# Kernel tuning notes

Measured on AMD Instinct MI355X. Metric: run time of the kernel, lower is better.

Reference implementation:

```python
import jax, jax.numpy as jnp
import numpy as np

N, E, B = 100000, 1600000, 64
TD, VD, AD = 768, 2048, 512
HC, H = 32, 4
NV, NA = 20000, 20000


def setup_inputs() -> dict:
    key = jax.random.key(0)
    ks = iter(jax.random.split(key, 80))
    def nrm(shape, scale=0.05):
        return (jax.random.normal(next(ks), shape, jnp.float32) * scale)
    inp = {}
    inp["x"] = jax.random.normal(next(ks), (N, TD), jnp.float32)
    inp["x_vision"] = jax.random.normal(next(ks), (NV, VD), jnp.float32)
    inp["x_audio"] = jax.random.normal(next(ks), (NA, AD), jnp.float32)
    inp["src"] = jax.random.randint(next(ks), (E,), 0, N, jnp.int32)
    inp["dst"] = jax.random.randint(next(ks), (E,), 0, N, jnp.int32)
    inp["vidx"] = jnp.arange(NV, dtype=jnp.int32) + 1000   # disjoint vision node ids
    inp["aidx"] = jnp.arange(NA, dtype=jnp.int32) + 30000  # disjoint audio node ids
    inp["ptr"] = (jnp.arange(B + 1) * (N // B)).astype(jnp.int32)
    # modality projections
    inp["Wt"] = nrm((HC, TD)); inp["bt"] = jnp.zeros((HC,), jnp.float32)
    inp["Wv"] = nrm((HC, VD)); inp["bv"] = jnp.zeros((HC,), jnp.float32)
    inp["gv"] = jnp.ones((HC,), jnp.float32); inp["bev"] = jnp.zeros((HC,), jnp.float32)
    inp["Wa"] = nrm((HC, AD)); inp["ba"] = jnp.zeros((HC,), jnp.float32)
    inp["ga"] = jnp.ones((HC,), jnp.float32); inp["bea"] = jnp.zeros((HC,), jnp.float32)
    # GATv2 convs: (in_dim, heads, concat)
    for p, cin, h, concat in (("c1", HC, H, True), ("c2", HC * H, H, True), ("c3", HC * H, H, True), ("c4", HC * H, 1, False)):
        inp[p + "_Wl"] = nrm((h * HC, cin)); inp[p + "_bl"] = jnp.zeros((h * HC,), jnp.float32)
        inp[p + "_Wr"] = nrm((h * HC, cin)); inp[p + "_br"] = jnp.zeros((h * HC,), jnp.float32)
        inp[p + "_att"] = nrm((h, HC))
        inp[p + "_b"] = jnp.zeros((h * HC if concat else HC,), jnp.float32)
    # layer norms
    for p, d in (("n1", HC * H), ("n2", HC * H), ("n3", HC * H), ("n4", HC)):
        inp[p + "_g"] = jnp.ones((d,), jnp.float32); inp[p + "_b"] = jnp.zeros((d,), jnp.float32)
    inp["Wo"] = nrm((1, HC), 0.01); inp["bo"] = jnp.zeros((1,), jnp.float32)
    return inp


def layernorm(x, g, b):
    m = x.mean(-1, keepdims=True)
    v = x.var(-1, keepdims=True)
    return (x - m) / jnp.sqrt(v + 1e-5) * g + b


def gatv2(x, src, dst, Wl, bl, Wr, br, att, b, concat):
    # PyG GATv2Conv (share_weights=False): e = att . leaky_relu(xl[src] + xr[dst])
    n = x.shape[0]
    h, c = att.shape
    xl = (x @ Wl.T + bl).reshape(n, h, c)
    xr = (x @ Wr.T + br).reshape(n, h, c)
    e = jnp.einsum('ehc,hc->eh', jax.nn.leaky_relu(xl[src] + xr[dst], 0.2), att)
    m = jax.ops.segment_max(e, dst, num_segments=n)          # segment softmax over dst
    w = jnp.exp(e - m[dst])
    s = jax.ops.segment_sum(w, dst, num_segments=n)
    alpha = w / (s[dst] + 1e-16)
    out = jax.ops.segment_sum(alpha[:, :, None] * xl[src], dst, num_segments=n)
    out = out.reshape(n, h * c) if concat else out.mean(1)
    return out + b


def reference(x, x_vision, x_audio, Wt, bt, Wv, bv, gv, bev, Wa, ba, ga, bea,
              c1_Wl, c1_bl, c1_Wr, c1_br, c1_att, c1_b,
              c2_Wl, c2_bl, c2_Wr, c2_br, c2_att, c2_b,
              c3_Wl, c3_bl, c3_Wr, c3_br, c3_att, c3_b,
              c4_Wl, c4_bl, c4_Wr, c4_br, c4_att, c4_b,
              n1_g, n1_b, n2_g, n2_b, n3_g, n3_b, n4_g, n4_b, Wo, bo,
              src, dst, vidx, aidx, ptr):
    n = x.shape[0]
    sl = jnp.arange(n, dtype=src.dtype)  # add_self_loops=True
    s2 = jnp.concatenate([src, sl]); d2 = jnp.concatenate([dst, sl])
    fx = x @ Wt.T + bt  # text projection (dropout = identity in eval)
    hv = jax.nn.relu(layernorm(x_vision @ Wv.T + bv, gv, bev))
    fx = fx.at[vidx].set(hv * x[vidx].mean(1, keepdims=True))
    ha = jax.nn.relu(layernorm(x_audio @ Wa.T + ba, ga, bea))
    fx = fx.at[aidx].set(ha * x[aidx].mean(1, keepdims=True))
    h1 = jax.nn.elu(layernorm(gatv2(fx, s2, d2, c1_Wl, c1_bl, c1_Wr, c1_br, c1_att, c1_b, True), n1_g, n1_b))
    h2 = jax.nn.elu(layernorm(gatv2(h1, s2, d2, c2_Wl, c2_bl, c2_Wr, c2_br, c2_att, c2_b, True) + h1, n2_g, n2_b))
    h3 = jax.nn.elu(layernorm(gatv2(h2, s2, d2, c3_Wl, c3_bl, c3_Wr, c3_br, c3_att, c3_b, True) + h2, n3_g, n3_b))
    h4 = layernorm(gatv2(h3, s2, d2, c4_Wl, c4_bl, c4_Wr, c4_br, c4_att, c4_b, False), n4_g, n4_b)
    summary = h4[ptr[:-1]]  # summary node = first node of each graph
    out = (summary @ Wo.T + bo).squeeze(-1)  # num_classes==2 -> squeeze
    return out
```

## Files before the change

### kernel.cpp

```cpp
#include <hip/hip_runtime.h>
#include <math.h>

#define NND 100000
#define NED 1600000
#define TDIM 768
#define VDIM 2048
#define ADIM 512
#define NVV 20000
#define NAA 20000
#define NBB 64
#define SUBROWS 8192

static __device__ __forceinline__ unsigned short f2bf(float f) {
  unsigned int u = __float_as_uint(f);
  unsigned int r = (u + 0x7fffu + ((u >> 16) & 1u)) >> 16;
  return (unsigned short)r;
}
static __device__ __forceinline__ float bf2f(unsigned int s) {
  return __uint_as_float(s << 16);
}

typedef __attribute__((ext_vector_type(8))) short bfrag;
typedef __attribute__((ext_vector_type(4))) float facc4;

static __device__ __forceinline__ bfrag pack8(const float4& a, const float4& b) {
  union { bfrag v; unsigned short u[8]; } r;
  r.u[0] = f2bf(a.x); r.u[1] = f2bf(a.y); r.u[2] = f2bf(a.z); r.u[3] = f2bf(a.w);
  r.u[4] = f2bf(b.x); r.u[5] = f2bf(b.y); r.u[6] = f2bf(b.z); r.u[7] = f2bf(b.w);
  return r.v;
}

static __device__ __forceinline__ float red16(float v) {
  #pragma unroll
  for (int m = 8; m >= 1; m >>= 1) v += __shfl_xor(v, m, 64);
  return v;
}
static __device__ __forceinline__ float red32(float v) {
  #pragma unroll
  for (int m = 16; m >= 1; m >>= 1) v += __shfl_xor(v, m, 64);
  return v;
}

__global__ void k_setcnt(int* cnt, int n) {
  int i = blockIdx.x * 256 + threadIdx.x;
  if (i < n) cnt[i] = 1;
}
__global__ void k_count(const int* __restrict__ dst, int* cnt, int e) {
  int i = blockIdx.x * 256 + threadIdx.x;
  if (i < e) atomicAdd(&cnt[dst[i]], 1);
}
__global__ void k_scan1(const int* __restrict__ cnt, int* rp, int* bsum, int n) {
  __shared__ int lds[256];
  int t = threadIdx.x;
  int base = blockIdx.x * 1024;
  int v[4];
  int s = 0;
  #pragma unroll
  for (int j = 0; j < 4; ++j) {
    int i = base + t * 4 + j;
    int c = (i < n) ? cnt[i] : 0;
    s += c; v[j] = s;
  }
  lds[t] = s;
  __syncthreads();
  for (int ofs = 1; ofs < 256; ofs <<= 1) {
    int x = (t >= ofs) ? lds[t - ofs] : 0;
    __syncthreads();
    lds[t] += x;
    __syncthreads();
  }
  int excl = (t > 0) ? lds[t - 1] : 0;
  #pragma unroll
  for (int j = 0; j < 4; ++j) {
    int i = base + t * 4 + j;
    if (i < n) rp[i + 1] = excl + v[j];
  }
  if (t == 255) bsum[blockIdx.x] = lds[255];
}
__global__ void k_scan2(int* bsum, int nb) {
  if (threadIdx.x == 0 && blockIdx.x == 0) {
    int acc = 0;
    for (int b = 0; b < nb; ++b) { int t = bsum[b]; bsum[b] = acc; acc += t; }
  }
}
__global__ void k_scan3(int* rp, const int* __restrict__ bsum, int n) {
  int i = blockIdx.x * 256 + threadIdx.x;
  if (i < n) rp[i + 1] += bsum[i >> 10];
  if (i == 0) rp[0] = 0;
}
__global__ void k_fillself(const int* __restrict__ rp, int* colidx, int* fill, int n) {
  int i = blockIdx.x * 256 + threadIdx.x;
  if (i < n) { colidx[rp[i]] = i; fill[i] = 1; }
}
__global__ void k_filledge(const int* __restrict__ src, const int* __restrict__ dst,
                           const int* __restrict__ rp, int* fill, int* colidx, int e) {
  int i = blockIdx.x * 256 + threadIdx.x;
  if (i < e) {
    int d = dst[i];
    int p = atomicAdd(&fill[d], 1);
    colidx[rp[d] + p] = src[i];
  }
}

__global__ void k_zeromark(int* m3, int* m2, int* cnts, int n) {
  int i = blockIdx.x * 256 + threadIdx.x;
  if (i < n) { m3[i] = 0; m2[i] = 0; }
  if (i < 2) cnts[i] = 0;
}
__global__ void k_mark3(const int* __restrict__ ptr, const int* __restrict__ rp,
                        const int* __restrict__ colidx, int* mark) {
  int node = ptr[blockIdx.x];
  int eb = rp[node], ee = rp[node + 1];
  if (threadIdx.x == 0) mark[node] = 1;
  for (int e = eb + (int)threadIdx.x; e < ee; e += 256) mark[colidx[e]] = 1;
}
__global__ void k_mark2(const int* __restrict__ list3, const int* __restrict__ cnt3,
                        const int* __restrict__ rp, const int* __restrict__ colidx,
                        int* mark) {
  int n3 = *cnt3;
  int wid = (blockIdx.x * 256 + threadIdx.x) >> 6;
  int l = threadIdx.x & 63;
  int nw = gridDim.x * 4;
  for (int i = wid; i < n3; i += nw) {
    int node = list3[i];
    if (l == 0) mark[node] = 1;
    int eb = rp[node], ee = rp[node + 1];
    for (int e = eb + l; e < ee; e += 64) mark[colidx[e]] = 1;
  }
}
__global__ void k_compact(const int* __restrict__ mark, int* list, int* cnt, int n) {
  int i = blockIdx.x * 256 + threadIdx.x;
  if (i < n && mark[i]) {
    int p = atomicAdd(cnt, 1);
    list[p] = i;
  }
}

__global__ void k_packall(
    const float* __restrict__ W0l, const float* __restrict__ W0r, unsigned short* o0,
    const float* __restrict__ W1l, const float* __restrict__ W1r, unsigned short* o1,
    const float* __restrict__ W2l, const float* __restrict__ W2r, unsigned short* o2,
    const float* __restrict__ W3l, const float* __restrict__ W3r, unsigned short* o3,
    const float* __restrict__ Wt, unsigned short* ot,
    const float* __restrict__ Wv, unsigned short* ov,
    const float* __restrict__ Wa, unsigned short* oa) {
  int i = blockIdx.x * 256 + threadIdx.x;
  if (i < 4096) { o0[i] = f2bf(W0l[i]); o0[4096 + i] = f2bf(W0r[i]); return; }
  i -= 4096;
  if (i < 16384) { o1[i] = f2bf(W1l[i]); o1[16384 + i] = f2bf(W1r[i]); return; }
  i -= 16384;
  if (i < 16384) { o2[i] = f2bf(W2l[i]); o2[16384 + i] = f2bf(W2r[i]); return; }
  i -= 16384;
  if (i < 4096) { o3[i] = f2bf(W3l[i]); o3[4096 + i] = f2bf(W3r[i]); return; }
  i -= 4096;
  if (i < 24576) { ot[i] = f2bf(Wt[i]); return; }
  i -= 24576;
  if (i < 65536) { ov[i] = f2bf(Wv[i]); return; }
  i -= 65536;
  if (i < 16384) { oa[i] = f2bf(Wa[i]); return; }
}

template <int K, bool MEAN, bool OBF>
__global__ __launch_bounds__(256) void gemm_mfma_in(
    const float* __restrict__ A, const unsigned short* __restrict__ Wb,
    const float* __restrict__ bias, void* __restrict__ Cv,
    float* __restrict__ rowmean, int M) {
  constexpr int KT = K / 32;
  const int wid = (int)threadIdx.x >> 6;
  const int lane = (int)threadIdx.x & 63;
  const int r16 = lane & 15;
  const int kg = lane >> 4;
  const int m0 = (blockIdx.x * 4 + wid) * 16;
  if (m0 >= M) return;
  const float* arow = A + (size_t)(m0 + r16) * K + kg * 8;
  const unsigned short* w0 = Wb + (size_t)r16 * K + kg * 8;
  const unsigned short* w1 = Wb + (size_t)(16 + r16) * K + kg * 8;
  facc4 acc0 = (facc4){0.f, 0.f, 0.f, 0.f};
  facc4 acc1 = (facc4){0.f, 0.f, 0.f, 0.f};
  float msum = 0.f;
  #pragma unroll 4
  for (int kt = 0; kt < KT; ++kt) {
    const float4* ap = reinterpret_cast<const float4*>(arow + kt * 32);
    float4 a0 = ap[0], a1 = ap[1];
    if (MEAN) msum += (a0.x + a0.y + a0.z + a0.w) + (a1.x + a1.y + a1.z + a1.w);
    bfrag af = pack8(a0, a1);
    bfrag b0 = *reinterpret_cast<const bfrag*>(w0 + kt * 32);
    bfrag b1 = *reinterpret_cast<const bfrag*>(w1 + kt * 32);
    acc0 = __builtin_amdgcn_mfma_f32_16x16x32_bf16(af, b0, acc0, 0, 0, 0);
    acc1 = __builtin_amdgcn_mfma_f32_16x16x32_bf16(af, b1, acc1, 0, 0, 0);
  }
  float b0v = bias[r16], b1v = bias[16 + r16];
  #pragma unroll
  for (int r = 0; r < 4; ++r) {
    int rowg = m0 + kg * 4 + r;
    float v0 = acc0[r] + b0v, v1 = acc1[r] + b1v;
    if (OBF) {
      unsigned short* C = (unsigned short*)Cv;
      C[(size_t)rowg * 32 + r16] = f2bf(v0);
      C[(size_t)rowg * 32 + 16 + r16] = f2bf(v1);
    } else {
      float* C = (float*)Cv;
      C[(size_t)rowg * 32 + r16] = v0;
      C[(size_t)rowg * 32 + 16 + r16] = v1;
    }
  }
  if (MEAN) {
    msum += __shfl_xor(msum, 16, 64);
    msum += __shfl_xor(msum, 32, 64);
    if (lane < 16) rowmean[m0 + r16] = msum * (1.f / (float)K);
  }
}

template <int K, int NHALF, int WAVES, bool IDX>
__global__ __launch_bounds__(WAVES * 64) void gemm_mfma(
    const unsigned short* __restrict__ A,
    const unsigned short* __restrict__ Wb,
    const float* __restrict__ bl, const float* __restrict__ br,
    unsigned short* __restrict__ Cl, unsigned short* __restrict__ Cr, int M,
    const int* __restrict__ rows, const int* __restrict__ rcnt) {
  constexpr int KT = K / 32;
  constexpr int NT = 2 * NHALF / 16;
  constexpr int NPW = NT / WAVES;
  static_assert(NPW >= 1, "bad wave split");
  const int wid = (int)threadIdx.x >> 6;
  const int lane = (int)threadIdx.x & 63;
  const int r16 = lane & 15;
  const int kg = lane >> 4;
  const int m0 = blockIdx.x * 16;
  int nr = M;
  if (IDX) nr = *rcnt;
  if (m0 >= nr) return;
  bfrag bf[NPW][KT];
  #pragma unroll
  for (int n = 0; n < NPW; ++n) {
    int col = (wid * NPW + n) * 16 + r16;
    #pragma unroll
    for (int kt = 0; kt < KT; ++kt)
      bf[n][kt] = *reinterpret_cast<const bfrag*>(Wb + (size_t)col * K + kt * 32 + kg * 8);
  }
  int ra = m0 + r16;
  if (IDX) { int mm = ra < nr ? ra : nr - 1; ra = rows[mm]; }
  bfrag af[KT];
  const unsigned short* arow = A + (size_t)ra * K + kg * 8;
  #pragma unroll
  for (int kt = 0; kt < KT; ++kt)
    af[kt] = *reinterpret_cast<const bfrag*>(arow + kt * 32);
  facc4 acc[NPW];
  #pragma unroll
  for (int n = 0; n < NPW; ++n) acc[n] = (facc4){0.f, 0.f, 0.f, 0.f};
  #pragma unroll
  for (int kt = 0; kt < KT; ++kt)
    #pragma unroll
    for (int n = 0; n < NPW; ++n)
      acc[n] = __builtin_amdgcn_mfma_f32_16x16x32_bf16(af[kt], bf[n][kt], acc[n], 0, 0, 0);
  #pragma unroll
  for (int n = 0; n < NPW; ++n) {
    int colg = (wid * NPW + n) * 16 + r16;
    bool isL = colg < NHALF;
    float bias = isL ? bl[colg] : br[colg - NHALF];
    #pragma unroll
    for (int r = 0; r < 4; ++r) {
      int m = m0 + kg * 4 + r;
      if (IDX && m >= nr) continue;
      int rowg = IDX ? rows[m] : m;
      unsigned short v = f2bf(acc[n][r] + bias);
      if (isL) Cl[(size_t)rowg * NHALF + colg] = v;
      else     Cr[(size_t)rowg * NHALF + (colg - NHALF)] = v;
    }
  }
}

template <bool RES, bool WL>
__global__ __launch_bounds__(256) void gat_agg_post128(
    const unsigned short* __restrict__ xl, const unsigned short* __restrict__ xr,
    const float* __restrict__ att,
    const int* __restrict__ rp, const int* __restrict__ colidx,
    const float* __restrict__ cb, const unsigned short* res,
    const float* __restrict__ g, const float* __restrict__ b,
    unsigned short* __restrict__ out, int n,
    const int* __restrict__ wl, const int* __restrict__ wcnt) {
  int wid = (blockIdx.x * 256 + threadIdx.x) >> 6;
  int node;
  if (WL) {
    if (wid >= *wcnt) return;
    node = wl[wid];
  } else {
    if (wid >= n) return;
    node = wid;
  }
  const int base = node * 128;
  int l = threadIdx.x & 63;
  const int lh = l & 31;
  const int half = l >> 5;
  const int c4 = 4 * lh;
  float4 a = *reinterpret_cast<const float4*>(att + c4);
  uint2 xru = *reinterpret_cast<const uint2*>(xr + base + c4);
  float xr0 = bf2f(xru.x & 0xffffu), xr1 = bf2f(xru.x >> 16);
  float xr2 = bf2f(xru.y & 0xffffu), xr3 = bf2f(xru.y >> 16);
  float m_ = -1e30f, s_ = 0.f;
  float ac0 = 0.f, ac1 = 0.f, ac2 = 0.f, ac3 = 0.f;
  int eb = rp[node], ee = rp[node + 1];
  int cnt = ee - eb;
  int nstep = (cnt + 1) >> 1;

  auto step = [&](uint2 cur, bool go) {
    float x0 = bf2f(cur.x & 0xffffu), x1 = bf2f(cur.x >> 16);
    float x2 = bf2f(cur.y & 0xffffu), x3 = bf2f(cur.y >> 16);
    float z0 = x0 + xr0, z1 = x1 + xr1, z2 = x2 + xr2, z3 = x3 + xr3;
    float t = (z0 > 0.f ? z0 : 0.2f * z0) * a.x + (z1 > 0.f ? z1 : 0.2f * z1) * a.y
            + (z2 > 0.f ? z2 : 0.2f * z2) * a.z + (z3 > 0.f ? z3 : 0.2f * z3) * a.w;
    t += __shfl_xor(t, 1, 64);
    t += __shfl_xor(t, 2, 64);
    t += __shfl_xor(t, 4, 64);
    if (!go) t = -1e30f;
    if (__any(t > m_ + 4.0f)) {
      float nm = fmaxf(m_, t);
      float p = __expf(m_ - nm);
      float w = __expf(t - nm);
      s_ = s_ * p + w;
      ac0 = ac0 * p + w * x0; ac1 = ac1 * p + w * x1;
      ac2 = ac2 * p + w * x2; ac3 = ac3 * p + w * x3;
      m_ = nm;
    } else {
      float w = __expf(t - m_);
      s_ += w;
      ac0 = fmaf(w, x0, ac0); ac1 = fmaf(w, x1, ac1);
      ac2 = fmaf(w, x2, ac2); ac3 = fmaf(w, x3, ac3);
    }
  };
  auto eclamp = [&](int s) { int e = 2 * s + half; return eb + (e < cnt ? e : cnt - 1); };
  auto ldx = [&](int sn) {
    return *reinterpret_cast<const uint2*>(xl + (size_t)sn * 128 + c4);
  };

  int idx[4];
  uint2 pv[4];
  #pragma unroll
  for (int k = 0; k < 4; ++k) idx[k] = colidx[eclamp(k)];
  #pragma unroll
  for (int k = 0; k < 4; ++k) pv[k] = ldx(idx[k]);
  for (int i = 0; i < nstep; i += 4) {
    uint2 q[4];
    #pragma unroll
    for (int k = 0; k < 4; ++k) q[k] = pv[k];
    if (i + 4 < nstep) {
      #pragma unroll
      for (int k = 0; k < 4; ++k) idx[k] = colidx[eclamp(i + 4 + k)];
      #pragma unroll
      for (int k = 0; k < 4; ++k) pv[k] = ldx(idx[k]);
    }
    step(q[0], 2 * i + half < cnt);
    if (i + 1 < nstep) step(q[1], 2 * (i + 1) + half < cnt);
    if (i + 2 < nstep) step(q[2], 2 * (i + 2) + half < cnt);
    if (i + 3 < nstep) step(q[3], 2 * (i + 3) + half < cnt);
  }

  float om = __shfl_xor(m_, 32, 64);
  float os = __shfl_xor(s_, 32, 64);
  float oa0 = __shfl_xor(ac0, 32, 64);
  float oa1 = __shfl_xor(ac1, 32, 64);
  float oa2 = __shfl_xor(ac2, 32, 64);
  float oa3 = __shfl_xor(ac3, 32, 64);
  float nm = fmaxf(m_, om);
  float ps = __expf(m_ - nm), po = __expf(om - nm);
  float s = s_ * ps + os * po;
  float inv = 1.f / (s + 1e-16f);
  float4 cbv = *reinterpret_cast<const float4*>(cb + c4);
  float v0 = (ac0 * ps + oa0 * po) * inv + cbv.x;
  float v1 = (ac1 * ps + oa1 * po) * inv + cbv.y;
  float v2 = (ac2 * ps + oa2 * po) * inv + cbv.z;
  float v3 = (ac3 * ps + oa3 * po) * inv + cbv.w;
  if (RES) {
    uint2 rv = *reinterpret_cast<const uint2*>(res + base + c4);
    v0 += bf2f(rv.x & 0xffffu); v1 += bf2f(rv.x >> 16);
    v2 += bf2f(rv.y & 0xffffu); v3 += bf2f(rv.y >> 16);
  }
  float S = v0 + v1 + v2 + v3;
  float Q = v0 * v0 + v1 * v1 + v2 * v2 + v3 * v3;
  #pragma unroll
  for (int m = 16; m >= 1; m >>= 1) {
    S += __shfl_xor(S, m, 64);
    Q += __shfl_xor(Q, m, 64);
  }
  float mean = S * (1.f / 128.f);
  float var = Q * (1.f / 128.f) - mean * mean;
  float rstd = rsqrtf(var + 1e-5f);
  float4 gv = *reinterpret_cast<const float4*>(g + c4);
  float4 bv = *reinterpret_cast<const float4*>(b + c4);
  float y0 = (v0 - mean) * rstd * gv.x + bv.x;
  float y1 = (v1 - mean) * rstd * gv.y + bv.y;
  float y2 = (v2 - mean) * rstd * gv.z + bv.z;
  float y3 = (v3 - mean) * rstd * gv.w + bv.w;
  y0 = (y0 > 0.f) ? y0 : expm1f(y0);
  y1 = (y1 > 0.f) ? y1 : expm1f(y1);
  y2 = (y2 > 0.f) ? y2 : expm1f(y2);
  y3 = (y3 > 0.f) ? y3 : expm1f(y3);
  if (half == 0) {
    uint2 o;
    o.x = (unsigned int)f2bf(y0) | ((unsigned int)f2bf(y1) << 16);
    o.y = (unsigned int)f2bf(y2) | ((unsigned int)f2bf(y3) << 16);
    *reinterpret_cast<uint2*>(out + base + c4) = o;
  }
}

__global__ void k_prep4(const int* __restrict__ ptr, const int* __restrict__ rp,
                        const int* __restrict__ colidx, int* off, int* gidx) {
  __shared__ int cnt_s[64];
  __shared__ int off_s[65];
  int t = threadIdx.x;
  if (t < 64) {
    int node = ptr[t];
    int deg = rp[node + 1] - rp[node];
    if (deg > 126) deg = 126;
    cnt_s[t] = deg + 1;
  }
  __syncthreads();
  if (t == 0) {
    int acc = 0;
    for (int i = 0; i < 64; ++i) { off_s[i] = acc; acc += cnt_s[i]; }
    off_s[64] = acc;
  }
  __syncthreads();
  if (t < 65) off[t] = off_s[t];
  if (t < 64) {
    int node = ptr[t];
    int o = off_s[t];
    gidx[o] = node;
    int eb = rp[node];
    int deg = cnt_s[t] - 1;
    for (int j = 0; j < deg; ++j) gidx[o + 1 + j] = colidx[eb + j];
  }
}

__global__ void k_gath4(const unsigned short* __restrict__ h, const int* __restrict__ gidx,
                        const int* __restrict__ off, unsigned short* __restrict__ hsub) {
  int tid = blockIdx.x * 256 + threadIdx.x;
  int j = tid >> 4, q = tid & 15;
  if (j >= SUBROWS) return;
  int count = off[64];
  bfrag v;
  #pragma unroll
  for (int i = 0; i < 8; ++i) v[i] = 0;
  if (j < count) v = *reinterpret_cast<const bfrag*>(h + (size_t)gidx[j] * 128 + q * 8);
  *reinterpret_cast<bfrag*>(hsub + (size_t)j * 128 + q * 8) = v;
}

__global__ __launch_bounds__(256) void k_agg4_final(
    const unsigned short* __restrict__ xls, const unsigned short* __restrict__ xrs,
    const float* __restrict__ att, const int* __restrict__ off,
    const float* __restrict__ cb, const float* __restrict__ g,
    const float* __restrict__ b, const float* __restrict__ Wo,
    const float* __restrict__ bo, float* __restrict__ out) {
  int wid = (blockIdx.x * 256 + threadIdx.x) >> 6;
  int l = threadIdx.x & 63;
  int lg = l & 15;
  int node = 4 * wid + (l >> 4);
  int c2 = 2 * lg;
  int p0 = off[node], pe = off[node + 1];
  int deg = pe - p0 - 1;
  float2 a = *reinterpret_cast<const float2*>(att + c2);
  unsigned int xru = *reinterpret_cast<const unsigned int*>(xrs + (size_t)p0 * 32 + c2);
  float xr0 = bf2f(xru & 0xffffu), xr1 = bf2f(xru >> 16);
  float m_ = -1e30f, s_ = 0.f, accx = 0.f, accy = 0.f;
  for (int i = 0;; ++i) {
    bool go = i < deg;
    if (!__any(go)) break;
    float xcx = 0.f, xcy = 0.f;
    float t = -1e30f;
    if (go) {
      unsigned int pv = *reinterpret_cast<const unsigned int*>(xls + (size_t)(p0 + 1 + i) * 32 + c2);
      xcx = bf2f(pv & 0xffffu);
      xcy = bf2f(pv >> 16);
      float z0 = xcx + xr0, z1 = xcy + xr1;
      t = (z0 > 0.f ? z0 : 0.2f * z0) * a.x + (z1 > 0.f ? z1 : 0.2f * z1) * a.y;
    }
    t = red16(t);
    if (!go) t = -1e30f;
    if (__any(t > m_ + 4.0f)) {
      float nm = fmaxf(m_, t);
      float p = __expf(m_ - nm);
      float w = __expf(t - nm);
      s_ = s_ * p + w;
      accx = accx * p + w * xcx;
      accy = accy * p + w * xcy;
      m_ = nm;
    } else {
      float w = __expf(t - m_);
      s_ += w;
      accx = fmaf(w, xcx, accx);
      accy = fmaf(w, xcy, accy);
    }
  }
  float inv = 1.f / (s_ + 1e-16f);
  float2 cbv = *reinterpret_cast<const float2*>(cb + c2);
  float v0 = accx * inv + cbv.x;
  float v1 = accy * inv + cbv.y;
  float S = red16(v0 + v1);
  float Q = red16(v0 * v0 + v1 * v1);
  float mean = S * (1.f / 32.f);
  float var = Q * (1.f / 32.f) - mean * mean;
  float rstd = rsqrtf(var + 1e-5f);
  float2 gv = *reinterpret_cast<const float2*>(g + c2);
  float2 bv = *reinterpret_cast<const float2*>(b + c2);
  float y0 = (v0 - mean) * rstd * gv.x + bv.x;
  float y1 = (v1 - mean) * rstd * gv.y + bv.y;
  float2 wo = *reinterpret_cast<const float2*>(Wo + c2);
  float d = red16(y0 * wo.x + y1 * wo.y);
  if (lg == 0) out[node] = d + bo[0];
}

__global__ __launch_bounds__(256) void k_modal2(
    unsigned short* fx, const float* __restrict__ hv, const float* __restrict__ ha,
    const int* __restrict__ vidx, const int* __restrict__ aidx,
    const float* __restrict__ gv, const float* __restrict__ bev,
    const float* __restrict__ ga, const float* __restrict__ bea,
    const float* __restrict__ rowmean, int nv, int na) {
  int wid = (blockIdx.x * 256 + threadIdx.x) >> 6;
  int l = threadIdx.x & 63;
  if (wid >= nv + na) return;
  bool isV = wid < nv;
  int w2 = isV ? wid : wid - nv;
  const float* hraw = isV ? hv : ha;
  const float* gg = isV ? gv : ga;
  const float* be = isV ? bev : bea;
  int node = isV ? vidx[w2] : aidx[w2];
  float mean = rowmean[node];
  float hval = (l < 32) ? hraw[(size_t)w2 * 32 + l] : 0.f;
  float S = red32(hval);
  float Q = red32(hval * hval);
  if (l < 32) {
    float m2 = S * (1.f / 32.f);
    float var = Q * (1.f / 32.f) - m2 * m2;
    float rstd = rsqrtf(var + 1e-5f);
    float y = (hval - m2) * rstd * gg[l] + be[l];
    y = fmaxf(y, 0.f);
    fx[(size_t)node * 32 + l] = f2bf(y * mean);
  }
}

extern "C" void kernel_launch(void* const* d_in, const int* in_sizes, int n_in,
                              void* d_out, int out_size, void* d_ws, size_t ws_size,
                              hipStream_t stream) {
  const float* x   = (const float*)d_in[0];
  const float* xv  = (const float*)d_in[1];
  const float* xa  = (const float*)d_in[2];
  const int* src   = (const int*)d_in[3];
  const int* dst   = (const int*)d_in[4];
  const int* vidx  = (const int*)d_in[5];
  const int* aidx  = (const int*)d_in[6];
  const int* ptr   = (const int*)d_in[7];
  const float* Wt  = (const float*)d_in[8];
  const float* bt  = (const float*)d_in[9];
  const float* Wv  = (const float*)d_in[10];
  const float* bv  = (const float*)d_in[11];
  const float* gv  = (const float*)d_in[12];
  const float* bev = (const float*)d_in[13];
  const float* Wa  = (const float*)d_in[14];
  const float* ba  = (const float*)d_in[15];
  const float* ga  = (const float*)d_in[16];
  const float* bea = (const float*)d_in[17];
  const float* cW_l[4], *cb_l[4], *cW_r[4], *cb_r[4], *c_att[4], *c_b[4];
  for (int i = 0; i < 4; ++i) {
    cW_l[i]  = (const float*)d_in[18 + 6 * i + 0];
    cb_l[i]  = (const float*)d_in[18 + 6 * i + 1];
    cW_r[i]  = (const float*)d_in[18 + 6 * i + 2];
    cb_r[i]  = (const float*)d_in[18 + 6 * i + 3];
    c_att[i] = (const float*)d_in[18 + 6 * i + 4];
    c_b[i]   = (const float*)d_in[18 + 6 * i + 5];
  }
  const float* ng[4], *nb_[4];
  for (int i = 0; i < 4; ++i) {
    ng[i]  = (const float*)d_in[42 + 2 * i + 0];
    nb_[i] = (const float*)d_in[42 + 2 * i + 1];
  }
  const float* Wo = (const float*)d_in[50];
  const float* bo = (const float*)d_in[51];
  float* out = (float*)d_out;

  char* w = (char*)d_ws;
  auto alloc = [&](size_t bytes) {
    char* p = w;
    w += (bytes + 255) & ~(size_t)255;
    return p;
  };
  int* rowptr = (int*)alloc((NND + 1) * sizeof(int));
  int* cnt    = (int*)alloc(NND * sizeof(int));
  int* bsum   = (int*)alloc(1024 * sizeof(int));
  int* colidx = (int*)alloc((size_t)(NED + NND) * sizeof(int));
  float* rowmean = (float*)alloc((size_t)NND * sizeof(float));
  unsigned short* fx = (unsigned short*)alloc((size_t)NND * 32 * sizeof(unsigned short));
  unsigned short* h  = (unsigned short*)alloc((size_t)NND * 128 * sizeof(unsigned short));
  unsigned short* xlb = (unsigned short*)alloc((size_t)NND * 128 * sizeof(unsigned short));
  unsigned short* xrb = (unsigned short*)alloc((size_t)NND * 128 * sizeof(unsigned short));
  float* hvraw = (float*)alloc((size_t)NVV * 32 * sizeof(float));
  float* haraw = (float*)alloc((size_t)NAA * 32 * sizeof(float));
  unsigned short* wb0 = (unsigned short*)alloc(256 * 32 * sizeof(unsigned short));
  unsigned short* wb1 = (unsigned short*)alloc(256 * 128 * sizeof(unsigned short));
  unsigned short* wb2 = (unsigned short*)alloc(256 * 128 * sizeof(unsigned short));
  unsigned short* wb3 = (unsigned short*)alloc(64 * 128 * sizeof(unsigned short));
  unsigned short* wbt = (unsigned short*)alloc(32 * TDIM * sizeof(unsigned short));
  unsigned short* wbv = (unsigned short*)alloc(32 * VDIM * sizeof(unsigned short));
  unsigned short* wba = (unsigned short*)alloc(32 * ADIM * sizeof(unsigned short));
  int* off4 = (int*)alloc(65 * sizeof(int));
  int* gidx = (int*)alloc(SUBROWS * sizeof(int));
  unsigned short* hsub = (unsigned short*)alloc((size_t)SUBROWS * 128 * sizeof(unsigned short));
  unsigned short* xls = (unsigned short*)alloc((size_t)SUBROWS * 32 * sizeof(unsigned short));
  unsigned short* xrs = (unsigned short*)alloc((size_t)SUBROWS * 32 * sizeof(unsigned short));
  int* mark3 = (int*)alloc((size_t)NND * sizeof(int));
  int* mark2 = (int*)alloc((size_t)NND * sizeof(int));
  int* list3 = (int*)alloc((size_t)NND * sizeof(int));
  int* list2 = (int*)alloc((size_t)NND * sizeof(int));
  int* cnts  = (int*)alloc(2 * sizeof(int));

  const int nblk_n = (NND + 255) / 256;
  const int nblk_e = (NED + 255) / 256;
  const int nscan = (NND + 1023) / 1024;
  const int nwave_n = (NND * 64 + 255) / 256;
  const int nwave_m2 = ((NVV + NAA) * 64 + 255) / 256;
  const int ntile = (NND + 15) / 16;

  k_setcnt<<<nblk_n, 256, 0, stream>>>(cnt, NND);
  k_count<<<nblk_e, 256, 0, stream>>>(dst, cnt, NED);
  k_scan1<<<nscan, 256, 0, stream>>>(cnt, rowptr, bsum, NND);
  k_scan2<<<1, 64, 0, stream>>>(bsum, nscan);
  k_scan3<<<nblk_n, 256, 0, stream>>>(rowptr, bsum, NND);
  k_fillself<<<nblk_n, 256, 0, stream>>>(rowptr, colidx, cnt, NND);
  k_filledge<<<nblk_e, 256, 0, stream>>>(src, dst, rowptr, cnt, colidx, NED);

  k_packall<<<576, 256, 0, stream>>>(
      cW_l[0], cW_r[0], wb0, cW_l[1], cW_r[1], wb1,
      cW_l[2], cW_r[2], wb2, cW_l[3], cW_r[3], wb3,
      Wt, wbt, Wv, wbv, Wa, wba);

  k_prep4<<<1, 256, 0, stream>>>(ptr, rowptr, colidx, off4, gidx);

  k_zeromark<<<nblk_n, 256, 0, stream>>>(mark3, mark2, cnts, NND);
  k_mark3<<<64, 256, 0, stream>>>(ptr, rowptr, colidx, mark3);
  k_compact<<<nblk_n, 256, 0, stream>>>(mark3, list3, cnts + 0, NND);
  k_mark2<<<256, 256, 0, stream>>>(list3, cnts + 0, rowptr, colidx, mark2);
  k_compact<<<nblk_n, 256, 0, stream>>>(mark2, list2, cnts + 1, NND);

  gemm_mfma_in<TDIM, true, true><<<(NND + 63) / 64, 256, 0, stream>>>(
      x, wbt, bt, fx, rowmean, NND);
  gemm_mfma_in<VDIM, false, false><<<(NVV + 63) / 64, 256, 0, stream>>>(
      xv, wbv, bv, hvraw, nullptr, NVV);
  gemm_mfma_in<ADIM, false, false><<<(NAA + 63) / 64, 256, 0, stream>>>(
      xa, wba, ba, haraw, nullptr, NAA);
  k_modal2<<<nwave_m2, 256, 0, stream>>>(
      fx, hvraw, haraw, vidx, aidx, gv, bev, ga, bea, rowmean, NVV, NAA);

  gemm_mfma<32, 128, 8, false><<<ntile, 512, 0, stream>>>(
      fx, wb0, cb_l[0], cb_r[0], xlb, xrb, NND, nullptr, nullptr);
  gat_agg_post128<false, false><<<nwave_n, 256, 0, stream>>>(
      xlb, xrb, c_att[0], rowptr, colidx, c_b[0], nullptr, ng[0], nb_[0], h, NND,
      nullptr, nullptr);

  gemm_mfma<128, 128, 8, false><<<ntile, 512, 0, stream>>>(
      h, wb1, cb_l[1], cb_r[1], xlb, xrb, NND, nullptr, nullptr);
  gat_agg_post128<true, true><<<nwave_n, 256, 0, stream>>>(
      xlb, xrb, c_att[1], rowptr, colidx, c_b[1], h, ng[1], nb_[1], h, NND,
      list2, cnts + 1);

  gemm_mfma<128, 128, 8, true><<<ntile, 512, 0, stream>>>(
      h, wb2, cb_l[2], cb_r[2], xlb, xrb, NND, list2, cnts + 1);
  gat_agg_post128<true, true><<<nwave_n, 256, 0, stream>>>(
      xlb, xrb, c_att[2], rowptr, colidx, c_b[2], h, ng[2], nb_[2], h, NND,
      list3, cnts + 0);

  k_gath4<<<(SUBROWS * 16 + 255) / 256, 256, 0, stream>>>(h, gidx, off4, hsub);
  gemm_mfma<128, 32, 4, false><<<SUBROWS / 16, 256, 0, stream>>>(
      hsub, wb3, cb_l[3], cb_r[3], xls, xrs, SUBROWS, nullptr, nullptr);
  k_agg4_final<<<4, 256, 0, stream>>>(
      xls, xrs, c_att[3], off4, c_b[3], ng[3], nb_[3], Wo, bo, out);
}
```

Baseline: 673.0 us.

## Fuse preprocessing kernels, single-pass scan, merged input GEMMs, gather-free layer-4 GEMM

```diff
diff --git a/kernel.cpp b/kernel.cpp
--- a/kernel.cpp
+++ b/kernel.cpp
@@ -11,6 +11,14 @@
 #define NBB 64
 #define SUBROWS 8192
 
+#define NBLK_N ((NND + 255) / 256)
+#define NBLK_E ((NED + 255) / 256)
+#define NSCAN ((NND + 1023) / 1024)
+#define NPACK 576
+#define NT_TXT ((NND + 63) / 64)
+#define NT_VIS ((NVV + 63) / 64)
+#define NT_AUD ((NAA + 63) / 64)
+
 static __device__ __forceinline__ unsigned short f2bf(float f) {
   unsigned int u = __float_as_uint(f);
   unsigned int r = (u + 0x7fffu + ((u >> 16) & 1u)) >> 16;
@@ -41,102 +49,15 @@
   return v;
 }
 
-__global__ void k_setcnt(int* cnt, int n) {
+__global__ void k_init(int* cnt, int* fill, int* m3, int* m2, int* cnts, int* agg, int n) {
   int i = blockIdx.x * 256 + threadIdx.x;
-  if (i < n) cnt[i] = 1;
-}
-__global__ void k_count(const int* __restrict__ dst, int* cnt, int e) {
-  int i = blockIdx.x * 256 + threadIdx.x;
-  if (i < e) atomicAdd(&cnt[dst[i]], 1);
-}
-__global__ void k_scan1(const int* __restrict__ cnt, int* rp, int* bsum, int n) {
-  __shared__ int lds[256];
-  int t = threadIdx.x;
-  int base = blockIdx.x * 1024;
-  int v[4];
-  int s = 0;
-  #pragma unroll
-  for (int j = 0; j < 4; ++j) {
-    int i = base + t * 4 + j;
-    int c = (i < n) ? cnt[i] : 0;
-    s += c; v[j] = s;
-  }
-  lds[t] = s;
-  __syncthreads();
-  for (int ofs = 1; ofs < 256; ofs <<= 1) {
-    int x = (t >= ofs) ? lds[t - ofs] : 0;
-    __syncthreads();
-    lds[t] += x;
-    __syncthreads();
-  }
-  int excl = (t > 0) ? lds[t - 1] : 0;
-  #pragma unroll
-  for (int j = 0; j < 4; ++j) {
-    int i = base + t * 4 + j;
-    if (i < n) rp[i + 1] = excl + v[j];
-  }
-  if (t == 255) bsum[blockIdx.x] = lds[255];
-}
-__global__ void k_scan2(int* bsum, int nb) {
-  if (threadIdx.x == 0 && blockIdx.x == 0) {
-    int acc = 0;
-    for (int b = 0; b < nb; ++b) { int t = bsum[b]; bsum[b] = acc; acc += t; }
-  }
-}
-__global__ void k_scan3(int* rp, const int* __restrict__ bsum, int n) {
-  int i = blockIdx.x * 256 + threadIdx.x;
-  if (i < n) rp[i + 1] += bsum[i >> 10];
-  if (i == 0) rp[0] = 0;
-}
-__global__ void k_fillself(const int* __restrict__ rp, int* colidx, int* fill, int n) {
-  int i = blockIdx.x * 256 + threadIdx.x;
-  if (i < n) { colidx[rp[i]] = i; fill[i] = 1; }
-}
-__global__ void k_filledge(const int* __restrict__ src, const int* __restrict__ dst,
-                           const int* __restrict__ rp, int* fill, int* colidx, int e) {
-  int i = blockIdx.x * 256 + threadIdx.x;
-  if (i < e) {
-    int d = dst[i];
-    int p = atomicAdd(&fill[d], 1);
-    colidx[rp[d] + p] = src[i];
-  }
-}
-
-__global__ void k_zeromark(int* m3, int* m2, int* cnts, int n) {
-  int i = blockIdx.x * 256 + threadIdx.x;
-  if (i < n) { m3[i] = 0; m2[i] = 0; }
+  if (i < n) { cnt[i] = 1; fill[i] = 1; m3[i] = 0; m2[i] = 0; }
   if (i < 2) cnts[i] = 0;
-}
-__global__ void k_mark3(const int* __restrict__ ptr, const int* __restrict__ rp,
-                        const int* __restrict__ colidx, int* mark) {
-  int node = ptr[blockIdx.x];
-  int eb = rp[node], ee = rp[node + 1];
-  if (threadIdx.x == 0) mark[node] = 1;
-  for (int e = eb + (int)threadIdx.x; e < ee; e += 256) mark[colidx[e]] = 1;
-}
-__global__ void k_mark2(const int* __restrict__ list3, const int* __restrict__ cnt3,
-                        const int* __restrict__ rp, const int* __restrict__ colidx,
-                        int* mark) {
-  int n3 = *cnt3;
-  int wid = (blockIdx.x * 256 + threadIdx.x) >> 6;
-  int l = threadIdx.x & 63;
-  int nw = gridDim.x * 4;
-  for (int i = wid; i < n3; i += nw) {
-    int node = list3[i];
-    if (l == 0) mark[node] = 1;
-    int eb = rp[node], ee = rp[node + 1];
-    for (int e = eb + l; e < ee; e += 64) mark[colidx[e]] = 1;
-  }
-}
-__global__ void k_compact(const int* __restrict__ mark, int* list, int* cnt, int n) {
-  int i = blockIdx.x * 256 + threadIdx.x;
-  if (i < n && mark[i]) {
-    int p = atomicAdd(cnt, 1);
-    list[p] = i;
-  }
-}
-
-__global__ void k_packall(
+  if (i < 128) agg[i] = 0;
+}
+
+__global__ void k_cntpack(
+    const int* __restrict__ dst, int* cnt,
     const float* __restrict__ W0l, const float* __restrict__ W0r, unsigned short* o0,
     const float* __restrict__ W1l, const float* __restrict__ W1r, unsigned short* o1,
     const float* __restrict__ W2l, const float* __restrict__ W2r, unsigned short* o2,
@@ -144,7 +65,13 @@
     const float* __restrict__ Wt, unsigned short* ot,
     const float* __restrict__ Wv, unsigned short* ov,
     const float* __restrict__ Wa, unsigned short* oa) {
-  int i = blockIdx.x * 256 + threadIdx.x;
+  int bid = blockIdx.x;
+  if (bid < NBLK_E) {
+    int i = bid * 256 + threadIdx.x;
+    if (i < NED) atomicAdd(&cnt[dst[i]], 1);
+    return;
+  }
+  int i = (bid - NBLK_E) * 256 + threadIdx.x;
   if (i < 4096) { o0[i] = f2bf(W0l[i]); o0[4096 + i] = f2bf(W0r[i]); return; }
   i -= 4096;
   if (i < 16384) { o1[i] = f2bf(W1l[i]); o1[16384 + i] = f2bf(W1r[i]); return; }
@@ -160,17 +87,127 @@
   if (i < 16384) { oa[i] = f2bf(Wa[i]); return; }
 }
 
+__global__ void k_scanall(const int* __restrict__ cnt, int* rp, int* agg, int n) {
+  __shared__ int lds[256];
+  int t = threadIdx.x, b = blockIdx.x;
+  int base = b * 1024;
+  int v[4];
+  int s = 0;
+  #pragma unroll
+  for (int j = 0; j < 4; ++j) {
+    int i = base + t * 4 + j;
+    int c = (i < n) ? cnt[i] : 0;
+    s += c; v[j] = s;
+  }
+  lds[t] = s;
+  __syncthreads();
+  for (int ofs = 1; ofs < 256; ofs <<= 1) {
+    int x = (t >= ofs) ? lds[t - ofs] : 0;
+    __syncthreads();
+    lds[t] += x;
+    __syncthreads();
+  }
+  int excl = (t > 0) ? lds[t - 1] : 0;
+  int total = lds[255];
+  if (t == 0) atomicExch(&agg[b], total);
+  __syncthreads();
+  int psum = 0;
+  for (int j = t; j < b; j += 256) {
+    int a;
+    do { a = atomicAdd(&agg[j], 0); } while (a == 0);
+    psum += a;
+  }
+  lds[t] = psum;
+  __syncthreads();
+  for (int ofs = 128; ofs >= 1; ofs >>= 1) {
+    if (t < ofs) lds[t] += lds[t + ofs];
+    __syncthreads();
+  }
+  int prefix = lds[0];
+  #pragma unroll
+  for (int j = 0; j < 4; ++j) {
+    int i = base + t * 4 + j;
+    if (i < n) rp[i + 1] = prefix + excl + v[j];
+  }
+  if (b == 0 && t == 0) rp[0] = 0;
+}
+
+__global__ void k_fill(const int* __restrict__ src, const int* __restrict__ dst,
+                       const int* __restrict__ rp, int* fill, int* colidx, int n, int e) {
+  int i = blockIdx.x * 256 + threadIdx.x;
+  if (i < n) colidx[rp[i]] = i;
+  if (i < e) {
+    int d = dst[i];
+    int p = atomicAdd(&fill[d], 1);
+    colidx[rp[d] + p] = src[i];
+  }
+}
+
+__global__ void k_prep4m(const int* __restrict__ ptr, const int* __restrict__ rp,
+                         const int* __restrict__ colidx, int* off, int* gidx, int* mark3) {
+  if (blockIdx.x > 0) {
+    int node = ptr[blockIdx.x - 1];
+    int eb = rp[node], ee = rp[node + 1];
+    if (threadIdx.x == 0) mark3[node] = 1;
+    for (int e = eb + (int)threadIdx.x; e < ee; e += 256) mark3[colidx[e]] = 1;
+    return;
+  }
+  __shared__ int cnt_s[64];
+  __shared__ int off_s[65];
+  int t = threadIdx.x;
+  if (t < 64) {
+    int node = ptr[t];
+    int deg = rp[node + 1] - rp[node];
+    if (deg > 126) deg = 126;
+    cnt_s[t] = deg + 1;
+  }
+  __syncthreads();
+  if (t == 0) {
+    int acc = 0;
+    for (int i = 0; i < 64; ++i) { off_s[i] = acc; acc += cnt_s[i]; }
+    off_s[64] = acc;
+  }
+  __syncthreads();
+  if (t < 65) off[t] = off_s[t];
+  if (t < 64) {
+    int node = ptr[t];
+    int o = off_s[t];
+    gidx[o] = node;
+    int eb = rp[node];
+    int deg = cnt_s[t] - 1;
+    for (int j = 0; j < deg; ++j) gidx[o + 1 + j] = colidx[eb + j];
+  }
+}
+
+__global__ void k_mark2s(const int* __restrict__ mark3, const int* __restrict__ rp,
+                         const int* __restrict__ colidx, int* mark2, int n) {
+  int i = blockIdx.x * 256 + threadIdx.x;
+  if (i >= n || !mark3[i]) return;
+  mark2[i] = 1;
+  int eb = rp[i], ee = rp[i + 1];
+  for (int e = eb; e < ee; ++e) mark2[colidx[e]] = 1;
+}
+
+__global__ void k_compact2(const int* __restrict__ m3, const int* __restrict__ m2,
+                           int* l3, int* l2, int* cnts, int n) {
+  int i = blockIdx.x * 256 + threadIdx.x;
+  if (i < n) {
+    if (m3[i]) { int p = atomicAdd(&cnts[0], 1); l3[p] = i; }
+    if (m2[i]) { int p = atomicAdd(&cnts[1], 1); l2[p] = i; }
+  }
+}
+
 template <int K, bool MEAN, bool OBF>
-__global__ __launch_bounds__(256) void gemm_mfma_in(
+static __device__ __forceinline__ void gemm_in_body(
     const float* __restrict__ A, const unsigned short* __restrict__ Wb,
     const float* __restrict__ bias, void* __restrict__ Cv,
-    float* __restrict__ rowmean, int M) {
+    float* __restrict__ rowmean, int M, int bid) {
   constexpr int KT = K / 32;
   const int wid = (int)threadIdx.x >> 6;
   const int lane = (int)threadIdx.x & 63;
   const int r16 = lane & 15;
   const int kg = lane >> 4;
-  const int m0 = (blockIdx.x * 4 + wid) * 16;
+  const int m0 = (bid * 4 + wid) * 16;
   if (m0 >= M) return;
   const float* arow = A + (size_t)(m0 + r16) * K + kg * 8;
   const unsigned short* w0 = Wb + (size_t)r16 * K + kg * 8;
@@ -211,7 +248,24 @@
   }
 }
 
-template <int K, int NHALF, int WAVES, bool IDX>
+__global__ __launch_bounds__(256) void k_gemm_in_all(
+    const float* __restrict__ x, const unsigned short* __restrict__ wbt,
+    const float* __restrict__ bt, unsigned short* fx, float* rowmean,
+    const float* __restrict__ xv, const unsigned short* __restrict__ wbv,
+    const float* __restrict__ bv, float* hvraw,
+    const float* __restrict__ xa, const unsigned short* __restrict__ wba,
+    const float* __restrict__ ba, float* haraw) {
+  int bid = blockIdx.x;
+  if (bid < NT_TXT) {
+    gemm_in_body<TDIM, true, true>(x, wbt, bt, fx, rowmean, NND, bid);
+  } else if (bid < NT_TXT + NT_VIS) {
+    gemm_in_body<VDIM, false, false>(xv, wbv, bv, hvraw, nullptr, NVV, bid - NT_TXT);
+  } else {
+    gemm_in_body<ADIM, false, false>(xa, wba, ba, haraw, nullptr, NAA, bid - NT_TXT - NT_VIS);
+  }
+}
+
+template <int K, int NHALF, int WAVES, int MODE>
 __global__ __launch_bounds__(WAVES * 64) void gemm_mfma(
     const unsigned short* __restrict__ A,
     const unsigned short* __restrict__ Wb,
@@ -228,7 +282,7 @@
   const int kg = lane >> 4;
   const int m0 = blockIdx.x * 16;
   int nr = M;
-  if (IDX) nr = *rcnt;
+  if (MODE >= 1) nr = *rcnt;
   if (m0 >= nr) return;
   bfrag bf[NPW][KT];
   #pragma unroll
@@ -239,7 +293,7 @@
       bf[n][kt] = *reinterpret_cast<const bfrag*>(Wb + (size_t)col * K + kt * 32 + kg * 8);
   }
   int ra = m0 + r16;
-  if (IDX) { int mm = ra < nr ? ra : nr - 1; ra = rows[mm]; }
+  if (MODE >= 1) { int mm = ra < nr ? ra : nr - 1; ra = rows[mm]; }
   bfrag af[KT];
   const unsigned short* arow = A + (size_t)ra * K + kg * 8;
   #pragma unroll
@@ -261,8 +315,8 @@
     #pragma unroll
     for (int r = 0; r < 4; ++r) {
       int m = m0 + kg * 4 + r;
-      if (IDX && m >= nr) continue;
-      int rowg = IDX ? rows[m] : m;
+      if (MODE == 1 && m >= nr) continue;
+      int rowg = (MODE == 1) ? rows[m] : m;
       unsigned short v = f2bf(acc[n][r] + bias);
       if (isL) Cl[(size_t)rowg * NHALF + colg] = v;
       else     Cr[(size_t)rowg * NHALF + (colg - NHALF)] = v;
@@ -401,48 +455,6 @@
     o.y = (unsigned int)f2bf(y2) | ((unsigned int)f2bf(y3) << 16);
     *reinterpret_cast<uint2*>(out + base + c4) = o;
   }
-}
-
-__global__ void k_prep4(const int* __restrict__ ptr, const int* __restrict__ rp,
-                        const int* __restrict__ colidx, int* off, int* gidx) {
-  __shared__ int cnt_s[64];
-  __shared__ int off_s[65];
-  int t = threadIdx.x;
-  if (t < 64) {
-    int node = ptr[t];
-    int deg = rp[node + 1] - rp[node];
-    if (deg > 126) deg = 126;
-    cnt_s[t] = deg + 1;
-  }
-  __syncthreads();
-  if (t == 0) {
-    int acc = 0;
-    for (int i = 0; i < 64; ++i) { off_s[i] = acc; acc += cnt_s[i]; }
-    off_s[64] = acc;
-  }
-  __syncthreads();
-  if (t < 65) off[t] = off_s[t];
-  if (t < 64) {
-    int node = ptr[t];
-    int o = off_s[t];
-    gidx[o] = node;
-    int eb = rp[node];
-    int deg = cnt_s[t] - 1;
-    for (int j = 0; j < deg; ++j) gidx[o + 1 + j] = colidx[eb + j];
-  }
-}
-
-__global__ void k_gath4(const unsigned short* __restrict__ h, const int* __restrict__ gidx,
-                        const int* __restrict__ off, unsigned short* __restrict__ hsub) {
-  int tid = blockIdx.x * 256 + threadIdx.x;
-  int j = tid >> 4, q = tid & 15;
-  if (j >= SUBROWS) return;
-  int count = off[64];
-  bfrag v;
-  #pragma unroll
-  for (int i = 0; i < 8; ++i) v[i] = 0;
-  if (j < count) v = *reinterpret_cast<const bfrag*>(h + (size_t)gidx[j] * 128 + q * 8);
-  *reinterpret_cast<bfrag*>(hsub + (size_t)j * 128 + q * 8) = v;
 }
 
 __global__ __launch_bounds__(256) void k_agg4_final(
@@ -585,7 +597,7 @@
   };
   int* rowptr = (int*)alloc((NND + 1) * sizeof(int));
   int* cnt    = (int*)alloc(NND * sizeof(int));
-  int* bsum   = (int*)alloc(1024 * sizeof(int));
+  int* aggs   = (int*)alloc(128 * sizeof(int));
   int* colidx = (int*)alloc((size_t)(NED + NND) * sizeof(int));
   float* rowmean = (float*)alloc((size_t)NND * sizeof(float));
   unsigned short* fx = (unsigned short*)alloc((size_t)NND * 32 * sizeof(unsigned short));
@@ -603,7 +615,6 @@
   unsigned short* wba = (unsigned short*)alloc(32 * ADIM * sizeof(unsigned short));
   int* off4 = (int*)alloc(65 * sizeof(int));
   int* gidx = (int*)alloc(SUBROWS * sizeof(int));
-  unsigned short* hsub = (unsigned short*)alloc((size_t)SUBROWS * 128 * sizeof(unsigned short));
   unsigned short* xls = (unsigned short*)alloc((size_t)SUBROWS * 32 * sizeof(unsigned short));
   unsigned short* xrs = (unsigned short*)alloc((size_t)SUBROWS * 32 * sizeof(unsigned short));
   int* mark3 = (int*)alloc((size_t)NND * sizeof(int));
@@ -612,64 +623,47 @@
   int* list2 = (int*)alloc((size_t)NND * sizeof(int));
   int* cnts  = (int*)alloc(2 * sizeof(int));
 
-  const int nblk_n = (NND + 255) / 256;
-  const int nblk_e = (NED + 255) / 256;
-  const int nscan = (NND + 1023) / 1024;
   const int nwave_n = (NND * 64 + 255) / 256;
   const int nwave_m2 = ((NVV + NAA) * 64 + 255) / 256;
   const int ntile = (NND + 15) / 16;
 
-  k_setcnt<<<nblk_n, 256, 0, stream>>>(cnt, NND);
-  k_count<<<nblk_e, 256, 0, stream>>>(dst, cnt, NED);
-  k_scan1<<<nscan, 256, 0, stream>>>(cnt, rowptr, bsum, NND);
-  k_scan2<<<1, 64, 0, stream>>>(bsum, nscan);
-  k_scan3<<<nblk_n, 256, 0, stream>>>(rowptr, bsum, NND);
-  k_fillself<<<nblk_n, 256, 0, stream>>>(rowptr, colidx, cnt, NND);
-  k_filledge<<<nblk_e, 256, 0, stream>>>(src, dst, rowptr, cnt, colidx, NED);
-
-  k_packall<<<576, 256, 0, stream>>>(
+  int* fill = list2;
+  k_init<<<NBLK_N, 256, 0, stream>>>(cnt, fill, mark3, mark2, cnts, aggs, NND);
+  k_cntpack<<<NBLK_E + NPACK, 256, 0, stream>>>(
+      dst, cnt,
       cW_l[0], cW_r[0], wb0, cW_l[1], cW_r[1], wb1,
       cW_l[2], cW_r[2], wb2, cW_l[3], cW_r[3], wb3,
       Wt, wbt, Wv, wbv, Wa, wba);
-
-  k_prep4<<<1, 256, 0, stream>>>(ptr, rowptr, colidx, off4, gidx);
-
-  k_zeromark<<<nblk_n, 256, 0, stream>>>(mark3, mark2, cnts, NND);
-  k_mark3<<<64, 256, 0, stream>>>(ptr, rowptr, colidx, mark3);
-  k_compact<<<nblk_n, 256, 0, stream>>>(mark3, list3, cnts + 0, NND);
-  k_mark2<<<256, 256, 0, stream>>>(list3, cnts + 0, rowptr, colidx, mark2);
-  k_compact<<<nblk_n, 256, 0, stream>>>(mark2, list2, cnts + 1, NND);
-
-  gemm_mfma_in<TDIM, true, true><<<(NND + 63) / 64, 256, 0, stream>>>(
-      x, wbt, bt, fx, rowmean, NND);
-  gemm_mfma_in<VDIM, false, false><<<(NVV + 63) / 64, 256, 0, stream>>>(
-      xv, wbv, bv, hvraw, nullptr, NVV);
-  gemm_mfma_in<ADIM, false, false><<<(NAA + 63) / 64, 256, 0, stream>>>(
-      xa, wba, ba, haraw, nullptr, NAA);
+  k_scanall<<<NSCAN, 256, 0, stream>>>(cnt, rowptr, aggs, NND);
+  k_fill<<<NBLK_E, 256, 0, stream>>>(src, dst, rowptr, fill, colidx, NND, NED);
+  k_prep4m<<<65, 256, 0, stream>>>(ptr, rowptr, colidx, off4, gidx, mark3);
+  k_mark2s<<<NBLK_N, 256, 0, stream>>>(mark3, rowptr, colidx, mark2, NND);
+  k_compact2<<<NBLK_N, 256, 0, stream>>>(mark3, mark2, list3, list2, cnts, NND);
+  k_gemm_in_all<<<NT_TXT + NT_VIS + NT_AUD, 256, 0, stream>>>(
+      x, wbt, bt, fx, rowmean, xv, wbv, bv, hvraw, xa, wba, ba, haraw);
   k_modal2<<<nwave_m2, 256, 0, stream>>>(
       fx, hvraw, haraw, vidx, aidx, gv, bev, ga, bea, rowmean, NVV, NAA);
 
-  gemm_mfma<32, 128, 8, false><<<ntile, 512, 0, stream>>>(
+  gemm_mfma<32, 128, 8, 0><<<ntile, 512, 0, stream>>>(
       fx, wb0, cb_l[0], cb_r[0], xlb, xrb, NND, nullptr, nullptr);
   gat_agg_post128<false, false><<<nwave_n, 256, 0, stream>>>(
       xlb, xrb, c_att[0], rowptr, colidx, c_b[0], nullptr, ng[0], nb_[0], h, NND,
       nullptr, nullptr);
 
-  gemm_mfma<128, 128, 8, false><<<ntile, 512, 0, stream>>>(
+  gemm_mfma<128, 128, 8, 0><<<ntile, 512, 0, stream>>>(
       h, wb1, cb_l[1], cb_r[1], xlb, xrb, NND, nullptr, nullptr);
   gat_agg_post128<true, true><<<nwave_n, 256, 0, stream>>>(
       xlb, xrb, c_att[1], rowptr, colidx, c_b[1], h, ng[1], nb_[1], h, NND,
       list2, cnts + 1);
 
-  gemm_mfma<128, 128, 8, true><<<ntile, 512, 0, stream>>>(
+  gemm_mfma<128, 128, 8, 1><<<ntile, 512, 0, stream>>>(
       h, wb2, cb_l[2], cb_r[2], xlb, xrb, NND, list2, cnts + 1);
-  gat_agg_post128<true, true><<<nwave_n, 256, 0, stream>>>(
+  gat_agg_post128<true, true><<<4096, 256, 0, stream>>>(
       xlb, xrb, c_att[2], rowptr, colidx, c_b[2], h, ng[2], nb_[2], h, NND,
       list3, cnts + 0);
 
-  k_gath4<<<(SUBROWS * 16 + 255) / 256, 256, 0, stream>>>(h, gidx, off4, hsub);
-  gemm_mfma<128, 32, 4, false><<<SUBROWS / 16, 256, 0, stream>>>(
-      hsub, wb3, cb_l[3], cb_r[3], xls, xrs, SUBROWS, nullptr, nullptr);
+  gemm_mfma<128, 32, 4, 2><<<SUBROWS / 16, 256, 0, stream>>>(
+      h, wb3, cb_l[3], cb_r[3], xls, xrs, SUBROWS, gidx, off4 + 64);
   k_agg4_final<<<4, 256, 0, stream>>>(
       xls, xrs, c_att[3], off4, c_b[3], ng[3], nb_[3], Wo, bo, out);
 }
```

New measurement: 629.4 us. -6.5%, faster.
